# Kernel tuning notes

Measured on AMD Instinct MI355X. Metric: run time of the kernel, lower is better.

The kernel has to match this reference:

```python
import jax, jax.numpy as jnp
import numpy as np
from jax import lax

HID = 512   # hidden_dim
DI = 1024   # d_inner = ssm_ratio * hidden_dim
N = 64      # ssm_d_state
R = 32      # dt_rank = ceil(512/16)
K = 4       # k_group
B, H, W = 4, 32, 32
MLP = 2048  # mlp_ratio * hidden_dim


def _ln(x, w, b):
    m = x.mean(-1, keepdims=True)
    v = ((x - m) ** 2).mean(-1, keepdims=True)
    return (x - m) / jnp.sqrt(v + 1e-5) * w + b


def setup_inputs() -> dict:
    key = jax.random.key(0)
    ks = jax.random.split(key, 12)
    rn = lambda k, s, sc: jax.random.normal(k, s, jnp.float32) * sc
    inp = {}
    inp["content"] = rn(ks[0], (B, H, W, HID), 1.0)
    inp["style"] = rn(ks[1], (B, H, W, HID), 1.0)
    inp["norm1_w"] = jnp.ones((HID,), jnp.float32)
    inp["norm1_b"] = jnp.zeros((HID,), jnp.float32)
    inp["in_proj_w"] = rn(ks[2], (HID, 2 * DI), HID ** -0.5)
    inp["conv_w"] = rn(ks[3], (DI, 1, 3, 3), 1.0 / 3.0)  # depthwise
    inp["conv_b"] = jnp.zeros((DI,), jnp.float32)
    inp["style_proj_w"] = rn(ks[4], (HID, K * (R + N)), HID ** -0.5)
    inp["content_proj_w"] = rn(ks[5], (DI, K * N), DI ** -0.5)
    inp["dt_projs_weight"] = rn(ks[6], (K, DI, R), R ** -0.5)
    inp["dt_projs_bias"] = rn(ks[7], (K, DI), 0.1)
    inp["A_logs"] = rn(ks[8], (K * DI, N), 0.1)
    inp["Ds"] = jnp.ones((K * DI,), jnp.float32)
    inp["out_proj_w"] = rn(ks[9], (DI, HID), DI ** -0.5)
    inp["norm2_w"] = jnp.ones((HID,), jnp.float32)
    inp["norm2_b"] = jnp.zeros((HID,), jnp.float32)
    inp["mlp_w1"] = rn(ks[10], (HID, MLP), HID ** -0.5)
    inp["mlp_b1"] = jnp.zeros((MLP,), jnp.float32)
    inp["mlp_w2"] = rn(ks[11], (MLP, HID), MLP ** -0.5)
    inp["mlp_b2"] = jnp.zeros((HID,), jnp.float32)
    return inp


def reference(content, style, norm1_w, norm1_b, in_proj_w, conv_w, conv_b,
              style_proj_w, content_proj_w, dt_projs_weight, dt_projs_bias,
              A_logs, Ds, out_proj_w, norm2_w, norm2_b,
              mlp_w1, mlp_b1, mlp_w2, mlp_b2):
    Bb, Hh, Ww, C = content.shape
    L = Hh * Ww
    res1 = content
    cn = _ln(content, norm1_w, norm1_b)
    sn = _ln(style, norm1_w, norm1_b)  # norm1 shared, as in source
    xz = cn @ in_proj_w                 # (B,H,W,2*DI)
    x, z = jnp.split(xz, 2, axis=-1)
    xc = x.transpose(0, 3, 1, 2)        # (B,DI,H,W)
    xconv = lax.conv_general_dilated(
        xc, conv_w, (1, 1), 'SAME', feature_group_count=DI,
        dimension_numbers=('NCHW', 'OIHW', 'NCHW')) + conv_b[None, :, None, None]
    xa = jax.nn.silu(xconv)             # (B,DI,H,W)
    # style-derived dt/B, content-derived C
    sp = (sn @ style_proj_w).reshape(Bb, L, K * (R + N))
    dts_rank, Bs = jnp.split(sp, [K * R], axis=-1)
    Cs = (xa.transpose(0, 2, 3, 1) @ content_proj_w).reshape(Bb, L, K * N)
    # cross_scan: 4 directions (raster, transposed raster, and their flips)
    xf = xa.reshape(Bb, DI, L)
    xt = xa.transpose(0, 1, 3, 2).reshape(Bb, DI, L)
    xs = jnp.stack([xf, xt, xf[..., ::-1], xt[..., ::-1]], axis=1)  # (B,K,DI,L)
    dts_rank = dts_rank.reshape(Bb, L, K, R).transpose(0, 2, 3, 1)   # (B,K,R,L)
    dts = jnp.einsum('bkrl,kdr->bkdl', dts_rank, dt_projs_weight)    # (B,K,DI,L)
    Bsm = Bs.reshape(Bb, L, K, N).transpose(0, 2, 3, 1)              # (B,K,N,L)
    Csm = Cs.reshape(Bb, L, K, N).transpose(0, 2, 3, 1)              # (B,K,N,L)
    A = -jnp.exp(A_logs.astype(jnp.float32)).reshape(K, DI, N)
    delta = jax.nn.softplus(dts + dt_projs_bias[None, :, :, None])   # (B,K,DI,L)
    # selective scan: h_t = exp(delta_t*A)*h_{t-1} + delta_t*B_t*u_t ; y_t = <h_t, C_t>
    def step(h, inpt):
        u_t, d_t, B_t, C_t = inpt  # (B,K,DI),(B,K,DI),(B,K,N),(B,K,N)
        h = jnp.exp(d_t[..., None] * A) * h + (d_t * u_t)[..., None] * B_t[:, :, None, :]
        y = jnp.einsum('bkdn,bkn->bkd', h, C_t)
        return h, y
    h0 = jnp.zeros((Bb, K, DI, N), jnp.float32)
    seq = (xs.transpose(3, 0, 1, 2), delta.transpose(3, 0, 1, 2),
           Bsm.transpose(3, 0, 1, 2), Csm.transpose(3, 0, 1, 2))
    _, ys = lax.scan(step, h0, seq)                                  # (L,B,K,DI)
    y_scan = ys.transpose(1, 2, 3, 0) + xs * Ds.reshape(K, DI)[None, :, :, None]
    # source sums the 4 directions without un-flipping (faithful)
    y = y_scan.reshape(Bb, K, DI, Hh, Ww).sum(1).transpose(0, 2, 3, 1)  # (B,H,W,DI)
    y = (y * z) @ out_proj_w
    x1 = res1 + y
    xn = _ln(x1, norm2_w, norm2_b)
    m = jax.nn.gelu(xn @ mlp_w1 + mlp_b1, approximate=False) @ mlp_w2 + mlp_b2
    return x1 + m
```

## Files before the change

kernel.cpp:

```cpp
#include <hip/hip_runtime.h>

#define B_ 4
#define Hh_ 32
#define Ww_ 32
#define L_ 1024
#define HID_ 512
#define DI_ 1024
#define N_ 64
#define R_ 32
#define K_ 4
#define MLP_ 2048

typedef __bf16 bf16x8 __attribute__((ext_vector_type(8)));
typedef float f32x4 __attribute__((ext_vector_type(4)));
typedef float v2f __attribute__((ext_vector_type(2)));

__device__ __forceinline__ unsigned short f2bf(float f) {
  unsigned int u = __builtin_bit_cast(unsigned int, f);
  return (unsigned short)((u + 0x7FFFu + ((u >> 16) & 1u)) >> 16);
}
__device__ __forceinline__ float bf2f(unsigned short h) {
  return __builtin_bit_cast(float, (unsigned int)h << 16);
}

__device__ __forceinline__ void gload16(const unsigned short* g, unsigned short* l) {
  __builtin_amdgcn_global_load_lds(
      (const __attribute__((address_space(1))) unsigned int*)g,
      (__attribute__((address_space(3))) unsigned int*)l, 16, 0, 0);
}

template <int CTRL>
__device__ __forceinline__ float dpp_add(float x) {
  int i = __builtin_bit_cast(int, x);
  int j = __builtin_amdgcn_update_dpp(i, i, CTRL, 0xF, 0xF, false);
  return x + __builtin_bit_cast(float, j);
}

__global__ __launch_bounds__(256) void transpose_all(
    const float* __restrict__ s0, const float* __restrict__ s1,
    const float* __restrict__ s2, const float* __restrict__ s3,
    const float* __restrict__ s4, const float* __restrict__ s5,
    unsigned short* __restrict__ t0, unsigned short* __restrict__ t1,
    unsigned short* __restrict__ t2, unsigned short* __restrict__ t3,
    unsigned short* __restrict__ t4, unsigned short* __restrict__ t5) {
  __shared__ float t[32][33];
  int bid = blockIdx.x;
  const float* src; unsigned short* dst; int K, N, bx, by;
  if (bid < 1024)      { src = s0; dst = t0; K = 512;  N = 2048; int r = bid;        bx = r & 63; by = r >> 6; }
  else if (bid < 1216) { src = s1; dst = t1; K = 512;  N = 384;  int r = bid - 1024; bx = r % 12; by = r / 12; }
  else if (bid < 1472) { src = s2; dst = t2; K = 1024; N = 256;  int r = bid - 1216; bx = r & 7;  by = r >> 3; }
  else if (bid < 1984) { src = s3; dst = t3; K = 1024; N = 512;  int r = bid - 1472; bx = r & 15; by = r >> 4; }
  else if (bid < 3008) { src = s4; dst = t4; K = 512;  N = 2048; int r = bid - 1984; bx = r & 63; by = r >> 6; }
  else                 { src = s5; dst = t5; K = 2048; N = 512;  int r = bid - 3008; bx = r & 15; by = r >> 4; }
  int nb = bx * 32, kb = by * 32;
  int tx = threadIdx.x & 31, ty = threadIdx.x >> 5;
  for (int r = ty; r < 32; r += 8) t[r][tx] = src[(size_t)(kb + r) * N + nb + tx];
  __syncthreads();
  for (int r = ty; r < 32; r += 8) dst[(size_t)(nb + r) * K + kb + tx] = f2bf(t[tx][r]);
}

__global__ __launch_bounds__(256) void ln_kernel(
    const float* __restrict__ in0, unsigned short* __restrict__ out0,
    const float* __restrict__ in1, unsigned short* __restrict__ out1,
    const float* __restrict__ w, const float* __restrict__ bb) {
  const float* in = blockIdx.y ? in1 : in0;
  unsigned short* out = blockIdx.y ? out1 : out0;
  int row = blockIdx.x * 4 + (threadIdx.x >> 6);
  int lane = threadIdx.x & 63;
  const float* p = in + (size_t)row * HID_;
  float4 v0 = *(const float4*)(p + lane * 4);
  float4 v1 = *(const float4*)(p + 256 + lane * 4);
  float s = v0.x + v0.y + v0.z + v0.w + v1.x + v1.y + v1.z + v1.w;
  float q = v0.x * v0.x + v0.y * v0.y + v0.z * v0.z + v0.w * v0.w +
            v1.x * v1.x + v1.y * v1.y + v1.z * v1.z + v1.w * v1.w;
  #pragma unroll
  for (int m = 1; m < 64; m <<= 1) { s += __shfl_xor(s, m, 64); q += __shfl_xor(q, m, 64); }
  float mean = s * (1.f / 512.f);
  float var = q * (1.f / 512.f) - mean * mean;
  float rstd = rsqrtf(var + 1e-5f);
  float4 w0 = *(const float4*)(w + lane * 4);
  float4 w1 = *(const float4*)(w + 256 + lane * 4);
  float4 b0 = *(const float4*)(bb + lane * 4);
  float4 b1 = *(const float4*)(bb + 256 + lane * 4);
  unsigned short* o = out + (size_t)row * HID_;
  ushort4 r0, r1;
  r0.x = f2bf((v0.x - mean) * rstd * w0.x + b0.x);
  r0.y = f2bf((v0.y - mean) * rstd * w0.y + b0.y);
  r0.z = f2bf((v0.z - mean) * rstd * w0.z + b0.z);
  r0.w = f2bf((v0.w - mean) * rstd * w0.w + b0.w);
  r1.x = f2bf((v1.x - mean) * rstd * w1.x + b1.x);
  r1.y = f2bf((v1.y - mean) * rstd * w1.y + b1.y);
  r1.z = f2bf((v1.z - mean) * rstd * w1.z + b1.z);
  r1.w = f2bf((v1.w - mean) * rstd * w1.w + b1.w);
  *(ushort4*)(o + lane * 4) = r0;
  *(ushort4*)(o + 256 + lane * 4) = r1;
}

#define BM 128
#define BN 128
#define BK 64

template <int EPI, int OUTBF>
__global__ __launch_bounds__(256) void gemm_kernel(
    const unsigned short* __restrict__ A, const unsigned short* __restrict__ BT,
    void* __restrict__ Cv, int M, int N, int K,
    const float* __restrict__ bias, const float* __restrict__ resid) {
  __shared__ __align__(16) unsigned short As[BM * BK];
  __shared__ __align__(16) unsigned short Bs[BN * BK];
  int tid = threadIdx.x;
  int lane = tid & 63, wv = tid >> 6;
  int wm = wv >> 1, wn = wv & 1;
  int nwg = gridDim.x * gridDim.y;
  int flat = blockIdx.y * gridDim.x + blockIdx.x;
  int swz = (flat & 7) * (nwg >> 3) + (flat >> 3);
  int bx = swz % gridDim.x, by = swz / gridDim.x;
  int m0 = by * BM, n0 = bx * BN;
  f32x4 acc[4][4] = {};
  int rowblk = lane >> 3;
  int sblk = (lane & 7) ^ rowblk;
  int rA = wm * 64 + (lane & 15);
  int rB = wn * 64 + (lane & 15);
  for (int k0 = 0; k0 < K; k0 += BK) {
    __syncthreads();
    #pragma unroll
    for (int it = 0; it < 4; ++it) {
      int r0 = wv * 32 + it * 8;
      gload16(A + (size_t)(m0 + r0 + rowblk) * K + k0 + sblk * 8, &As[r0 * BK]);
      gload16(BT + (size_t)(n0 + r0 + rowblk) * K + k0 + sblk * 8, &Bs[r0 * BK]);
    }
    __syncthreads();
    #pragma unroll
    for (int kx = 0; kx < 2; ++kx) {
      int bidx = (lane >> 4) + kx * 4;
      bf16x8 fa[4], fb[4];
      #pragma unroll
      for (int i = 0; i < 4; ++i) {
        int ra = rA + i * 16;
        int rb = rB + i * 16;
        fa[i] = *(const bf16x8*)&As[ra * BK + ((bidx ^ (ra & 7)) << 3)];
        fb[i] = *(const bf16x8*)&Bs[rb * BK + ((bidx ^ (rb & 7)) << 3)];
      }
      #pragma unroll
      for (int i = 0; i < 4; ++i)
        #pragma unroll
        for (int j = 0; j < 4; ++j)
          acc[i][j] = __builtin_amdgcn_mfma_f32_16x16x32_bf16(fa[i], fb[j], acc[i][j], 0, 0, 0);
    }
  }
  int crow0 = m0 + wm * 64 + (lane >> 4) * 4, ccol0 = n0 + wn * 64 + (lane & 15);
  #pragma unroll
  for (int i = 0; i < 4; ++i) {
    #pragma unroll
    for (int j = 0; j < 4; ++j) {
      int col = ccol0 + j * 16;
      #pragma unroll
      for (int r = 0; r < 4; ++r) {
        int row = crow0 + i * 16 + r;
        float v = acc[i][j][r];
        if (EPI == 1) v += resid[(size_t)row * N + col];
        if (EPI == 2) { v += bias[col]; v = 0.5f * v * (1.f + erff(v * 0.70710678f)); }
        if (EPI == 3) v += bias[col] + resid[(size_t)row * N + col];
        if (OUTBF) ((unsigned short*)Cv)[(size_t)row * N + col] = f2bf(v);
        else       ((float*)Cv)[(size_t)row * N + col] = v;
      }
    }
  }
}

template <int EPI, int OUTBF>
__global__ __launch_bounds__(256) void gemm64_kernel(
    const unsigned short* __restrict__ A, const unsigned short* __restrict__ BT,
    void* __restrict__ Cv, int M, int N, int K,
    const float* __restrict__ bias, const float* __restrict__ resid) {
  __shared__ __align__(16) unsigned short As[64 * BK];
  __shared__ __align__(16) unsigned short Bs[128 * BK];
  int tid = threadIdx.x;
  int lane = tid & 63, wv = tid >> 6;
  int wm = wv >> 1, wn = wv & 1;
  int nwg = gridDim.x * gridDim.y;
  int flat = blockIdx.y * gridDim.x + blockIdx.x;
  int swz = (flat & 7) * (nwg >> 3) + (flat >> 3);
  int bx = swz % gridDim.x, by = swz / gridDim.x;
  int m0 = by * 64, n0 = bx * BN;
  f32x4 acc[2][4] = {};
  int rowblk = lane >> 3;
  int sblk = (lane & 7) ^ rowblk;
  int rA = wm * 32 + (lane & 15);
  int rB = wn * 64 + (lane & 15);
  for (int k0 = 0; k0 < K; k0 += BK) {
    __syncthreads();
    #pragma unroll
    for (int it = 0; it < 2; ++it) {
      int r0 = wv * 16 + it * 8;
      gload16(A + (size_t)(m0 + r0 + rowblk) * K + k0 + sblk * 8, &As[r0 * BK]);
    }
    #pragma unroll
    for (int it = 0; it < 4; ++it) {
      int r0 = wv * 32 + it * 8;
      gload16(BT + (size_t)(n0 + r0 + rowblk) * K + k0 + sblk * 8, &Bs[r0 * BK]);
    }
    __syncthreads();
    #pragma unroll
    for (int kx = 0; kx < 2; ++kx) {
      int bidx = (lane >> 4) + kx * 4;
      bf16x8 fa[2], fb[4];
      #pragma unroll
      for (int i = 0; i < 2; ++i) {
        int ra = rA + i * 16;
        fa[i] = *(const bf16x8*)&As[ra * BK + ((bidx ^ (ra & 7)) << 3)];
      }
      #pragma unroll
      for (int j = 0; j < 4; ++j) {
        int rb = rB + j * 16;
        fb[j] = *(const bf16x8*)&Bs[rb * BK + ((bidx ^ (rb & 7)) << 3)];
      }
      #pragma unroll
      for (int i = 0; i < 2; ++i)
        #pragma unroll
        for (int j = 0; j < 4; ++j)
          acc[i][j] = __builtin_amdgcn_mfma_f32_16x16x32_bf16(fa[i], fb[j], acc[i][j], 0, 0, 0);
    }
  }
  int crow0 = m0 + wm * 32 + (lane >> 4) * 4, ccol0 = n0 + wn * 64 + (lane & 15);
  #pragma unroll
  for (int i = 0; i < 2; ++i) {
    #pragma unroll
    for (int j = 0; j < 4; ++j) {
      int col = ccol0 + j * 16;
      #pragma unroll
      for (int r = 0; r < 4; ++r) {
        int row = crow0 + i * 16 + r;
        float v = acc[i][j][r];
        if (EPI == 1) v += resid[(size_t)row * N + col];
        if (EPI == 2) { v += bias[col]; v = 0.5f * v * (1.f + erff(v * 0.70710678f)); }
        if (EPI == 3) v += bias[col] + resid[(size_t)row * N + col];
        if (OUTBF) ((unsigned short*)Cv)[(size_t)row * N + col] = f2bf(v);
        else       ((float*)Cv)[(size_t)row * N + col] = v;
      }
    }
  }
}

__global__ __launch_bounds__(256) void conv_kernel(
    const unsigned short* __restrict__ xz, const float* __restrict__ cw,
    const float* __restrict__ cb, unsigned short* __restrict__ xa) {
  int idx = blockIdx.x * 256 + threadIdx.x;
  int d = idx & (DI_ - 1);
  int l = (idx >> 10) & (L_ - 1);
  int b = idx >> 20;
  int hh = l >> 5, ww = l & 31;
  float acc = cb[d];
  #pragma unroll
  for (int dh = -1; dh <= 1; ++dh) {
    int y = hh + dh;
    if ((unsigned)y >= 32u) continue;
    #pragma unroll
    for (int dw = -1; dw <= 1; ++dw) {
      int x = ww + dw;
      if ((unsigned)x >= 32u) continue;
      acc = fmaf(bf2f(xz[((size_t)b * L_ + y * 32 + x) * (2 * DI_) + d]),
                 cw[d * 9 + (dh + 1) * 3 + (dw + 1)], acc);
    }
  }
  float sv = acc / (1.f + __expf(-acc));
  xa[idx] = f2bf(sv);
}

__global__ __launch_bounds__(256) void delta_kernel(
    const float* __restrict__ sp, const float* __restrict__ dtw,
    const float* __restrict__ dtb, unsigned short* __restrict__ delta) {
  int bk = blockIdx.x;
  int b = bk >> 2, k = bk & 3;
  int dc = blockIdx.y * 256;
  int l0 = blockIdx.z * 128;
  __shared__ float wl[32 * 257];
  __shared__ float rl[128 * 32];
  int tid = threadIdx.x;
  for (int i = tid; i < 256 * 32; i += 256) {
    int dl = i >> 5, r = i & 31;
    wl[r * 257 + dl] = dtw[((size_t)k * DI_ + dc + dl) * R_ + r];
  }
  for (int i = tid; i < 128 * 32; i += 256) {
    int ll = i >> 5, r = i & 31;
    rl[ll * 32 + r] = sp[((size_t)b * L_ + l0 + ll) * 384 + k * R_ + r];
  }
  __syncthreads();
  float bias = dtb[k * DI_ + dc + tid];
  for (int ll = 0; ll < 128; ++ll) {
    float acc = bias;
    #pragma unroll
    for (int r = 0; r < 32; ++r)
      acc = fmaf(rl[ll * 32 + r], wl[r * 257 + tid], acc);
    float dlt = (acc > 15.f) ? acc : log1pf(__expf(acc));
    delta[(((size_t)(b * 4 + k) * L_) + l0 + ll) * DI_ + dc + tid] = f2bf(dlt);
  }
}

#define CH 16
#define NCH (L_ / CH)
#define DLP 36
#define YQP 6
__global__ __launch_bounds__(512) void scan_kernel(
    unsigned short* __restrict__ ybuf, const unsigned short* __restrict__ xa,
    const float* __restrict__ sp, const float* __restrict__ Cs,
    const unsigned short* __restrict__ dltb,
    const float* __restrict__ A_logs, const float* __restrict__ Ds) {
  int dblk = blockIdx.x;
  int k = blockIdx.y, b = blockIdx.z;
  int tid = threadIdx.x, lane = tid & 63, wv = tid >> 6;
  int dg = lane >> 4, ng = lane & 15;
  int qp = (lane >> 2) & 3;
  int wd = wv * 4 + dg;
  int gd = k * DI_ + dblk * 32 + wd;
  v2f a2p[2], h2[2];
  #pragma unroll
  for (int j = 0; j < 2; ++j) {
    a2p[j].x = -__expf(A_logs[(size_t)gd * N_ + ng * 4 + 2 * j]) * 1.44269504f;
    a2p[j].y = -__expf(A_logs[(size_t)gd * N_ + ng * 4 + 2 * j + 1]) * 1.44269504f;
    h2[j].x = 0.f; h2[j].y = 0.f;
  }

  __shared__ float Bsh[2][CH][64];
  __shared__ float Csh[2][CH][64];
  __shared__ float DLU[2][32][DLP];
  __shared__ float yq[CH][32][YQP];
  __shared__ float dsh[32];

  const size_t spB = (size_t)b * L_ * 384 + 128 + k * 64;
  const size_t csB = (size_t)b * L_ * 256 + k * 64;
  const size_t dlB = ((size_t)(b * 4 + k) * L_) * DI_ + dblk * 32;
  const size_t xaB = (size_t)b * L_ * DI_ + dblk * 32;

  if (tid < 32) dsh[tid] = Ds[k * DI_ + dblk * 32 + tid];

  int liS = tid >> 5, js = tid & 31;
  int liE = tid >> 5, dd = tid & 31;
  auto posf = [&](int l) {
    int lr = 1023 - l;
    return (k == 0) ? l
         : (k == 1) ? ((l & 31) * 32 + (l >> 5))
         : (k == 2) ? lr
                    : ((lr & 31) * 32 + (lr >> 5));
  };

  {
    *(float2*)&Bsh[0][liS][js * 2] = *(const float2*)(sp + spB + (size_t)liS * 384 + js * 2);
    *(float2*)&Csh[0][liS][js * 2] = *(const float2*)(Cs + csB + (size_t)liS * 256 + js * 2);
    float2 p;
    p.x = bf2f(dltb[dlB + (size_t)liS * DI_ + js]);
    p.y = bf2f(xa[xaB + (size_t)posf(liS) * DI_ + js]);
    *(float2*)&DLU[0][js][liS * 2] = p;
  }
  __syncthreads();

  int cur = 0;
  for (int c = 0; c < NCH; ++c) {
    float2 pB, pC;
    unsigned short pD, pU;
    if (c < NCH - 1) {
      int lb = (c + 1) * CH + liS;
      pB = *(const float2*)(sp + spB + (size_t)lb * 384 + js * 2);
      pC = *(const float2*)(Cs + csB + (size_t)lb * 256 + js * 2);
      pD = dltb[dlB + (size_t)lb * DI_ + js];
      pU = xa[xaB + (size_t)posf(lb) * DI_ + js];
    }
    #pragma unroll
    for (int li2 = 0; li2 < CH; li2 += 2) {
      f32x4 duq = *(const f32x4*)&DLU[cur][wd][li2 * 2];
      #pragma unroll
      for (int s = 0; s < 2; ++s) {
        int li = li2 + s;
        float dlt = s ? duq[2] : duq[0];
        float u   = s ? duq[3] : duq[1];
        float du = dlt * u;
        f32x4 bq = *(const f32x4*)&Bsh[cur][li][ng * 4];
        f32x4 cq = *(const f32x4*)&Csh[cur][li][ng * 4];
        v2f b01 = __builtin_shufflevector(bq, bq, 0, 1);
        v2f b23 = __builtin_shufflevector(bq, bq, 2, 3);
        v2f c01 = __builtin_shufflevector(cq, cq, 0, 1);
        v2f c23 = __builtin_shufflevector(cq, cq, 2, 3);
        v2f dlt2; dlt2.x = dlt; dlt2.y = dlt;
        v2f du2;  du2.x = du;  du2.y = du;
        v2f arg0 = dlt2 * a2p[0];
        v2f arg1 = dlt2 * a2p[1];
        v2f e0, e1;
        e0.x = __builtin_amdgcn_exp2f(arg0.x);
        e0.y = __builtin_amdgcn_exp2f(arg0.y);
        e1.x = __builtin_amdgcn_exp2f(arg1.x);
        e1.y = __builtin_amdgcn_exp2f(arg1.y);
        h2[0] = e0 * h2[0] + du2 * b01;
        h2[1] = e1 * h2[1] + du2 * b23;
        v2f yv = h2[0] * c01 + h2[1] * c23;
        float yp = yv.x + yv.y;
        yp = dpp_add<0xB1>(yp);
        yp = dpp_add<0x4E>(yp);
        yq[li][wd][qp] = yp;
      }
    }
    __syncthreads();
    {
      float2 q01 = *(const float2*)&yq[liE][dd][0];
      float2 q23 = *(const float2*)&yq[liE][dd][2];
      float y = (q01.x + q01.y) + (q23.x + q23.y);
      float u = DLU[cur][dd][liE * 2 + 1];
      y = fmaf(u, dsh[dd], y);
      ybuf[dlB + (size_t)(c * CH + liE) * DI_ + dd] = f2bf(y);
    }
    if (c < NCH - 1) {
      int nxt = cur ^ 1;
      *(float2*)&Bsh[nxt][liS][js * 2] = pB;
      *(float2*)&Csh[nxt][liS][js * 2] = pC;
      float2 p; p.x = bf2f(pD); p.y = bf2f(pU);
      *(float2*)&DLU[nxt][js][liS * 2] = p;
    }
    __syncthreads();
    cur ^= 1;
  }
}

__global__ __launch_bounds__(256) void fuse_ygz(
    const unsigned short* __restrict__ yk, const unsigned short* __restrict__ xz,
    unsigned short* __restrict__ ygz) {
  size_t i = ((size_t)blockIdx.x * 256 + threadIdx.x) * 8;
  size_t b = i >> 20, ld = i & ((1u << 20) - 1);
  float acc[8] = {};
  #pragma unroll
  for (int k = 0; k < 4; ++k) {
    uint4 v = *(const uint4*)(yk + ((size_t)(b * 4 + k) << 20) + ld);
    unsigned int w[4] = {v.x, v.y, v.z, v.w};
    #pragma unroll
    for (int t = 0; t < 4; ++t) {
      acc[t * 2 + 0] += __builtin_bit_cast(float, w[t] << 16);
      acc[t * 2 + 1] += __builtin_bit_cast(float, w[t] & 0xFFFF0000u);
    }
  }
  uint4 zv = *(const uint4*)(xz + (i >> 10) * (2 * DI_) + DI_ + (i & (DI_ - 1)));
  unsigned int zw[4] = {zv.x, zv.y, zv.z, zv.w};
  float z[8];
  #pragma unroll
  for (int t = 0; t < 4; ++t) {
    z[t * 2 + 0] = __builtin_bit_cast(float, zw[t] << 16);
    z[t * 2 + 1] = __builtin_bit_cast(float, zw[t] & 0xFFFF0000u);
  }
  uint4 o;
  o.x = (unsigned int)f2bf(acc[0] * z[0]) | ((unsigned int)f2bf(acc[1] * z[1]) << 16);
  o.y = (unsigned int)f2bf(acc[2] * z[2]) | ((unsigned int)f2bf(acc[3] * z[3]) << 16);
  o.z = (unsigned int)f2bf(acc[4] * z[4]) | ((unsigned int)f2bf(acc[5] * z[5]) << 16);
  o.w = (unsigned int)f2bf(acc[6] * z[6]) | ((unsigned int)f2bf(acc[7] * z[7]) << 16);
  *(uint4*)(ygz + i) = o;
}

extern "C" void kernel_launch(void* const* d_in, const int* in_sizes, int n_in,
                              void* d_out, int out_size, void* d_ws, size_t ws_size,
                              hipStream_t stream) {
  (void)in_sizes; (void)n_in; (void)out_size; (void)ws_size;
  const float* content   = (const float*)d_in[0];
  const float* style     = (const float*)d_in[1];
  const float* norm1_w   = (const float*)d_in[2];
  const float* norm1_b   = (const float*)d_in[3];
  const float* in_proj_w = (const float*)d_in[4];
  const float* conv_w    = (const float*)d_in[5];
  const float* conv_b    = (const float*)d_in[6];
  const float* style_proj_w   = (const float*)d_in[7];
  const float* content_proj_w = (const float*)d_in[8];
  const float* dtw       = (const float*)d_in[9];
  const float* dtb       = (const float*)d_in[10];
  const float* A_logs    = (const float*)d_in[11];
  const float* Ds        = (const float*)d_in[12];
  const float* out_proj_w = (const float*)d_in[13];
  const float* norm2_w   = (const float*)d_in[14];
  const float* norm2_b   = (const float*)d_in[15];
  const float* mlp_w1    = (const float*)d_in[16];
  const float* mlp_b1    = (const float*)d_in[17];
  const float* mlp_w2    = (const float*)d_in[18];
  const float* mlp_b2    = (const float*)d_in[19];
  float* out = (float*)d_out;

  float* ws = (float*)d_ws;
  const size_t ROWS = (size_t)B_ * L_;
  const size_t SCAN_ELEMS = (size_t)B_ * K_ * L_ * DI_;
  size_t o = 0;
  unsigned short* cn  = (unsigned short*)(ws + o); o += ROWS * HID_ / 2;
  unsigned short* sn  = (unsigned short*)(ws + o); o += ROWS * HID_ / 2;
  unsigned short* xn  = (unsigned short*)(ws + o); o += ROWS * HID_ / 2;
  unsigned short* xz  = (unsigned short*)(ws + o); o += ROWS * 2 * DI_ / 2;
  float* sp    = ws + o; o += ROWS * 384;
  unsigned short* xa = (unsigned short*)(ws + o); o += ROWS * DI_ / 2;
  float* csb   = ws + o; o += ROWS * 256;
  float* x1    = ws + o; o += ROWS * HID_;
  unsigned short* dltb = (unsigned short*)(ws + o); o += SCAN_ELEMS / 2;
  unsigned short* ybuf = (unsigned short*)(ws + o); o += SCAN_ELEMS / 2;
  unsigned short* ygz  = (unsigned short*)(ws + o); o += ROWS * DI_ / 2;
  unsigned short* wt = (unsigned short*)(ws + o);
  unsigned short* inpT = wt;
  unsigned short* styT = inpT + 2048 * 512;
  unsigned short* conT = styT + 384 * 512;
  unsigned short* outT = conT + 256 * 1024;
  unsigned short* w1T  = outT + 512 * 1024;
  unsigned short* w2T  = w1T + 2048 * 512;
  unsigned short* hmid = ybuf;

  transpose_all<<<4032, 256, 0, stream>>>(
      in_proj_w, style_proj_w, content_proj_w, out_proj_w, mlp_w1, mlp_w2,
      inpT, styT, conT, outT, w1T, w2T);

  ln_kernel<<<dim3(ROWS / 4, 2), 256, 0, stream>>>(content, cn, style, sn, norm1_w, norm1_b);

  gemm_kernel<0, 1><<<dim3(2048 / BN, ROWS / BM), 256, 0, stream>>>(
      cn, inpT, xz, ROWS, 2048, 512, nullptr, nullptr);
  gemm64_kernel<0, 0><<<dim3(384 / BN, ROWS / 64), 256, 0, stream>>>(
      sn, styT, sp, ROWS, 384, 512, nullptr, nullptr);
  conv_kernel<<<(ROWS * DI_) / 256, 256, 0, stream>>>(xz, conv_w, conv_b, xa);
  gemm64_kernel<0, 0><<<dim3(256 / BN, ROWS / 64), 256, 0, stream>>>(
      xa, conT, csb, ROWS, 256, 1024, nullptr, nullptr);
  delta_kernel<<<dim3(B_ * K_, DI_ / 256, L_ / 128), 256, 0, stream>>>(sp, dtw, dtb, dltb);
  scan_kernel<<<dim3(DI_ / 32, K_, B_), 512, 0, stream>>>(
      ybuf, xa, sp, csb, dltb, A_logs, Ds);
  fuse_ygz<<<(ROWS * DI_) / (256 * 8), 256, 0, stream>>>(ybuf, xz, ygz);
  gemm64_kernel<1, 0><<<dim3(512 / BN, ROWS / 64), 256, 0, stream>>>(
      ygz, outT, x1, ROWS, 512, 1024, nullptr, content);
  ln_kernel<<<dim3(ROWS / 4, 1), 256, 0, stream>>>(x1, xn, nullptr, nullptr, norm2_w, norm2_b);
  gemm_kernel<2, 1><<<dim3(2048 / BN, ROWS / BM), 256, 0, stream>>>(
      xn, w1T, hmid, ROWS, 2048, 512, mlp_b1, nullptr);
  gemm64_kernel<3, 0><<<dim3(512 / BN, ROWS / 64), 256, 0, stream>>>(
      hmid, w2T, out, ROWS, 512, 2048, mlp_b2, x1);
}
```

Baseline: 464.0 us.

## Compute delta projection with bf16 MFMA and store B/C projections as bf16

Replaces the scalar FP32 delta_kernel with an MFMA-based GEMM (dtgemm_kernel) over bf16 copies of the style projection and dt weights, with the softplus fused into its epilogue. The style and content projection GEMMs now write bf16 output, and the scan kernel reads packed bf16 B/C values into a single interleaved shared-memory buffer. This cuts FMA work in the delta computation and halves the memory traffic for the B/C inputs, at the cost of lower precision for B, C and dt inputs plus an extra cast kernel for the dt weights.

```diff
diff --git a/kernel.cpp b/kernel.cpp
--- a/kernel.cpp
+++ b/kernel.cpp
@@ -21,6 +21,12 @@
 }
 __device__ __forceinline__ float bf2f(unsigned short h) {
   return __builtin_bit_cast(float, (unsigned int)h << 16);
+}
+__device__ __forceinline__ v2f bfp2v(unsigned int u) {
+  v2f r;
+  r.x = __builtin_bit_cast(float, u << 16);
+  r.y = __builtin_bit_cast(float, u & 0xFFFF0000u);
+  return r;
 }
 
 __device__ __forceinline__ void gload16(const unsigned short* g, unsigned short* l) {
@@ -57,6 +63,14 @@
   for (int r = ty; r < 32; r += 8) t[r][tx] = src[(size_t)(kb + r) * N + nb + tx];
   __syncthreads();
   for (int r = ty; r < 32; r += 8) dst[(size_t)(nb + r) * K + kb + tx] = f2bf(t[tx][r]);
+}
+
+__global__ __launch_bounds__(256) void cast_bf(
+    const float* __restrict__ src, unsigned short* __restrict__ dst) {
+  int i = (blockIdx.x * 256 + threadIdx.x) * 4;
+  float4 v = *(const float4*)(src + i);
+  ushort4 o = {f2bf(v.x), f2bf(v.y), f2bf(v.z), f2bf(v.w)};
+  *(ushort4*)(dst + i) = o;
 }
 
 __global__ __launch_bounds__(256) void ln_kernel(
@@ -241,6 +255,59 @@
   }
 }
 
+__global__ __launch_bounds__(256) void dtgemm_kernel(
+    const unsigned short* __restrict__ sp, const unsigned short* __restrict__ dtwB,
+    const float* __restrict__ dtb, unsigned short* __restrict__ delta) {
+  int kq = blockIdx.z;
+  int m0 = blockIdx.y * 64, n0 = blockIdx.x * 128;
+  __shared__ __align__(16) unsigned short As[64 * 32];
+  __shared__ __align__(16) unsigned short Bs[128 * 32];
+  int tid = threadIdx.x, lane = tid & 63, wv = tid >> 6;
+  int wm = wv >> 1, wn = wv & 1;
+  {
+    int r = tid >> 2, c = (tid & 3) * 8;
+    *(uint4*)&As[r * 32 + c] = *(const uint4*)(sp + (size_t)(m0 + r) * 384 + kq * 32 + c);
+  }
+  {
+    int r = tid >> 1, c = (tid & 1) * 16;
+    const unsigned short* p = dtwB + (size_t)(kq * DI_ + n0 + r) * 32 + c;
+    *(uint4*)&Bs[r * 32 + c] = *(const uint4*)(p);
+    *(uint4*)&Bs[r * 32 + c + 8] = *(const uint4*)(p + 8);
+  }
+  __syncthreads();
+  int kk = (lane >> 4) * 8;
+  int rA = wm * 32 + (lane & 15);
+  int rB = wn * 64 + (lane & 15);
+  f32x4 acc[2][4] = {};
+  bf16x8 fa[2], fb[4];
+  #pragma unroll
+  for (int i = 0; i < 2; ++i) fa[i] = *(const bf16x8*)&As[(rA + i * 16) * 32 + kk];
+  #pragma unroll
+  for (int j = 0; j < 4; ++j) fb[j] = *(const bf16x8*)&Bs[(rB + j * 16) * 32 + kk];
+  #pragma unroll
+  for (int i = 0; i < 2; ++i)
+    #pragma unroll
+    for (int j = 0; j < 4; ++j)
+      acc[i][j] = __builtin_amdgcn_mfma_f32_16x16x32_bf16(fa[i], fb[j], acc[i][j], 0, 0, 0);
+  int crow0 = m0 + wm * 32 + (lane >> 4) * 4, ccol0 = n0 + wn * 64 + (lane & 15);
+  #pragma unroll
+  for (int i = 0; i < 2; ++i) {
+    #pragma unroll
+    for (int j = 0; j < 4; ++j) {
+      int col = ccol0 + j * 16;
+      float bias = dtb[kq * DI_ + col];
+      #pragma unroll
+      for (int r = 0; r < 4; ++r) {
+        int row = crow0 + i * 16 + r;
+        float v = acc[i][j][r] + bias;
+        v = (v > 15.f) ? v : log1pf(__expf(v));
+        int bb = row >> 10, l = row & 1023;
+        delta[(((size_t)(bb * 4 + kq)) << 20) + ((size_t)l << 10) + col] = f2bf(v);
+      }
+    }
+  }
+}
+
 __global__ __launch_bounds__(256) void conv_kernel(
     const unsigned short* __restrict__ xz, const float* __restrict__ cw,
     const float* __restrict__ cb, unsigned short* __restrict__ xa) {
@@ -266,43 +333,13 @@
   xa[idx] = f2bf(sv);
 }
 
-__global__ __launch_bounds__(256) void delta_kernel(
-    const float* __restrict__ sp, const float* __restrict__ dtw,
-    const float* __restrict__ dtb, unsigned short* __restrict__ delta) {
-  int bk = blockIdx.x;
-  int b = bk >> 2, k = bk & 3;
-  int dc = blockIdx.y * 256;
-  int l0 = blockIdx.z * 128;
-  __shared__ float wl[32 * 257];
-  __shared__ float rl[128 * 32];
-  int tid = threadIdx.x;
-  for (int i = tid; i < 256 * 32; i += 256) {
-    int dl = i >> 5, r = i & 31;
-    wl[r * 257 + dl] = dtw[((size_t)k * DI_ + dc + dl) * R_ + r];
-  }
-  for (int i = tid; i < 128 * 32; i += 256) {
-    int ll = i >> 5, r = i & 31;
-    rl[ll * 32 + r] = sp[((size_t)b * L_ + l0 + ll) * 384 + k * R_ + r];
-  }
-  __syncthreads();
-  float bias = dtb[k * DI_ + dc + tid];
-  for (int ll = 0; ll < 128; ++ll) {
-    float acc = bias;
-    #pragma unroll
-    for (int r = 0; r < 32; ++r)
-      acc = fmaf(rl[ll * 32 + r], wl[r * 257 + tid], acc);
-    float dlt = (acc > 15.f) ? acc : log1pf(__expf(acc));
-    delta[(((size_t)(b * 4 + k) * L_) + l0 + ll) * DI_ + dc + tid] = f2bf(dlt);
-  }
-}
-
 #define CH 16
 #define NCH (L_ / CH)
 #define DLP 36
 #define YQP 6
 __global__ __launch_bounds__(512) void scan_kernel(
     unsigned short* __restrict__ ybuf, const unsigned short* __restrict__ xa,
-    const float* __restrict__ sp, const float* __restrict__ Cs,
+    const unsigned short* __restrict__ sp, const unsigned short* __restrict__ Cs,
     const unsigned short* __restrict__ dltb,
     const float* __restrict__ A_logs, const float* __restrict__ Ds) {
   int dblk = blockIdx.x;
@@ -320,8 +357,7 @@
     h2[j].x = 0.f; h2[j].y = 0.f;
   }
 
-  __shared__ float Bsh[2][CH][64];
-  __shared__ float Csh[2][CH][64];
+  __shared__ __align__(16) unsigned short BCsh[2][CH][16][8];
   __shared__ float DLU[2][32][DLP];
   __shared__ float yq[CH][32][YQP];
   __shared__ float dsh[32];
@@ -334,6 +370,7 @@
   if (tid < 32) dsh[tid] = Ds[k * DI_ + dblk * 32 + tid];
 
   int liS = tid >> 5, js = tid & 31;
+  int gS = js >> 1, oS = (js & 1) * 2;
   int liE = tid >> 5, dd = tid & 31;
   auto posf = [&](int l) {
     int lr = 1023 - l;
@@ -344,8 +381,10 @@
   };
 
   {
-    *(float2*)&Bsh[0][liS][js * 2] = *(const float2*)(sp + spB + (size_t)liS * 384 + js * 2);
-    *(float2*)&Csh[0][liS][js * 2] = *(const float2*)(Cs + csB + (size_t)liS * 256 + js * 2);
+    unsigned int pB = *(const unsigned int*)(sp + spB + (size_t)liS * 384 + js * 2);
+    unsigned int pC = *(const unsigned int*)(Cs + csB + (size_t)liS * 256 + js * 2);
+    *(unsigned int*)&BCsh[0][liS][gS][oS] = pB;
+    *(unsigned int*)&BCsh[0][liS][gS][4 + oS] = pC;
     float2 p;
     p.x = bf2f(dltb[dlB + (size_t)liS * DI_ + js]);
     p.y = bf2f(xa[xaB + (size_t)posf(liS) * DI_ + js]);
@@ -355,12 +394,12 @@
 
   int cur = 0;
   for (int c = 0; c < NCH; ++c) {
-    float2 pB, pC;
+    unsigned int pB, pC;
     unsigned short pD, pU;
     if (c < NCH - 1) {
       int lb = (c + 1) * CH + liS;
-      pB = *(const float2*)(sp + spB + (size_t)lb * 384 + js * 2);
-      pC = *(const float2*)(Cs + csB + (size_t)lb * 256 + js * 2);
+      pB = *(const unsigned int*)(sp + spB + (size_t)lb * 384 + js * 2);
+      pC = *(const unsigned int*)(Cs + csB + (size_t)lb * 256 + js * 2);
       pD = dltb[dlB + (size_t)lb * DI_ + js];
       pU = xa[xaB + (size_t)posf(lb) * DI_ + js];
     }
@@ -373,12 +412,11 @@
         float dlt = s ? duq[2] : duq[0];
         float u   = s ? duq[3] : duq[1];
         float du = dlt * u;
-        f32x4 bq = *(const f32x4*)&Bsh[cur][li][ng * 4];
-        f32x4 cq = *(const f32x4*)&Csh[cur][li][ng * 4];
-        v2f b01 = __builtin_shufflevector(bq, bq, 0, 1);
-        v2f b23 = __builtin_shufflevector(bq, bq, 2, 3);
-        v2f c01 = __builtin_shufflevector(cq, cq, 0, 1);
-        v2f c23 = __builtin_shufflevector(cq, cq, 2, 3);
+        uint4 bc = *(const uint4*)&BCsh[cur][li][ng][0];
+        v2f b01 = bfp2v(bc.x);
+        v2f b23 = bfp2v(bc.y);
+        v2f c01 = bfp2v(bc.z);
+        v2f c23 = bfp2v(bc.w);
         v2f dlt2; dlt2.x = dlt; dlt2.y = dlt;
         v2f du2;  du2.x = du;  du2.y = du;
         v2f arg0 = dlt2 * a2p[0];
@@ -408,8 +446,8 @@
     }
     if (c < NCH - 1) {
       int nxt = cur ^ 1;
-      *(float2*)&Bsh[nxt][liS][js * 2] = pB;
-      *(float2*)&Csh[nxt][liS][js * 2] = pC;
+      *(unsigned int*)&BCsh[nxt][liS][gS][oS] = pB;
+      *(unsigned int*)&BCsh[nxt][liS][gS][4 + oS] = pC;
       float2 p; p.x = bf2f(pD); p.y = bf2f(pU);
       *(float2*)&DLU[nxt][js][liS * 2] = p;
     }
@@ -484,9 +522,9 @@
   unsigned short* sn  = (unsigned short*)(ws + o); o += ROWS * HID_ / 2;
   unsigned short* xn  = (unsigned short*)(ws + o); o += ROWS * HID_ / 2;
   unsigned short* xz  = (unsigned short*)(ws + o); o += ROWS * 2 * DI_ / 2;
-  float* sp    = ws + o; o += ROWS * 384;
-  unsigned short* xa = (unsigned short*)(ws + o); o += ROWS * DI_ / 2;
-  float* csb   = ws + o; o += ROWS * 256;
+  unsigned short* sp  = (unsigned short*)(ws + o); o += ROWS * 384 / 2;
+  unsigned short* xa  = (unsigned short*)(ws + o); o += ROWS * DI_ / 2;
+  unsigned short* csb = (unsigned short*)(ws + o); o += ROWS * 256 / 2;
   float* x1    = ws + o; o += ROWS * HID_;
   unsigned short* dltb = (unsigned short*)(ws + o); o += SCAN_ELEMS / 2;
   unsigned short* ybuf = (unsigned short*)(ws + o); o += SCAN_ELEMS / 2;
@@ -498,22 +536,24 @@
   unsigned short* outT = conT + 256 * 1024;
   unsigned short* w1T  = outT + 512 * 1024;
   unsigned short* w2T  = w1T + 2048 * 512;
+  unsigned short* dtwB = w2T + 512 * 2048;
   unsigned short* hmid = ybuf;
 
   transpose_all<<<4032, 256, 0, stream>>>(
       in_proj_w, style_proj_w, content_proj_w, out_proj_w, mlp_w1, mlp_w2,
       inpT, styT, conT, outT, w1T, w2T);
+  cast_bf<<<(K_ * DI_ * R_) / 1024, 256, 0, stream>>>(dtw, dtwB);
 
   ln_kernel<<<dim3(ROWS / 4, 2), 256, 0, stream>>>(content, cn, style, sn, norm1_w, norm1_b);
 
   gemm_kernel<0, 1><<<dim3(2048 / BN, ROWS / BM), 256, 0, stream>>>(
       cn, inpT, xz, ROWS, 2048, 512, nullptr, nullptr);
-  gemm64_kernel<0, 0><<<dim3(384 / BN, ROWS / 64), 256, 0, stream>>>(
+  gemm64_kernel<0, 1><<<dim3(384 / BN, ROWS / 64), 256, 0, stream>>>(
       sn, styT, sp, ROWS, 384, 512, nullptr, nullptr);
   conv_kernel<<<(ROWS * DI_) / 256, 256, 0, stream>>>(xz, conv_w, conv_b, xa);
-  gemm64_kernel<0, 0><<<dim3(256 / BN, ROWS / 64), 256, 0, stream>>>(
+  gemm64_kernel<0, 1><<<dim3(256 / BN, ROWS / 64), 256, 0, stream>>>(
       xa, conT, csb, ROWS, 256, 1024, nullptr, nullptr);
-  delta_kernel<<<dim3(B_ * K_, DI_ / 256, L_ / 128), 256, 0, stream>>>(sp, dtw, dtb, dltb);
+  dtgemm_kernel<<<dim3(DI_ / 128, ROWS / 64, K_), 256, 0, stream>>>(sp, dtwB, dtb, dltb);
   scan_kernel<<<dim3(DI_ / 32, K_, B_), 512, 0, stream>>>(
       ybuf, xa, sp, csb, dltb, A_logs, Ds);
   fuse_ygz<<<(ROWS * DI_) / (256 * 8), 256, 0, stream>>>(ybuf, xz, ygz);
```

New measurement: 484.9 us. 1.05x slower.
